# Kernel tuning notes

Measured on AMD Instinct MI355X. Metric: run time of the kernel, lower is better.

Reference implementation:

```python
import jax, jax.numpy as jnp
import numpy as np

NORM_EPS = 1e-5
NUM_HEAD = 16
DIM_HEAD = 32
DIM_HIDDEN = 512
DIM_POS = 2
N, S = 4, 8192


def setup_inputs() -> dict:
    key = jax.random.key(0)
    ks = jax.random.split(key, 16)
    d = DIM_HIDDEN
    inp = {
        "Q": jax.random.normal(ks[0], (N, S, d), jnp.float32),
        "K": jax.random.normal(ks[1], (N, S, d), jnp.float32),
        "V": jax.random.normal(ks[2], (N, S, d), jnp.float32),
        "position": jax.random.uniform(ks[3], (N, S, DIM_POS), jnp.float32),
        "W_Q": jax.random.normal(ks[4], (d, d), jnp.float32) * (1.0 / np.sqrt(d)),
        "W_K": jax.random.normal(ks[5], (d, d), jnp.float32) * (1.0 / np.sqrt(d)),
        "W_V": jax.random.normal(ks[6], (d, d), jnp.float32) * (1.0 / np.sqrt(d)),
        "b_Q": jnp.zeros((d,), jnp.float32),
        "b_K": jnp.zeros((d,), jnp.float32),
        "b_V": jnp.zeros((d,), jnp.float32),
        "ln_w_K": jnp.ones((NUM_HEAD, DIM_HEAD), jnp.float32),
        "ln_b_K": jnp.zeros((NUM_HEAD, DIM_HEAD), jnp.float32),
        "ln_w_V": jnp.ones((NUM_HEAD, DIM_HEAD), jnp.float32),
        "ln_b_V": jnp.zeros((NUM_HEAD, DIM_HEAD), jnp.float32),
        # torch Linear(dim_hidden + dim_position*num_head, dim_hidden): weight [out, in]
        "fc_W": jax.random.normal(ks[7], (d, d + DIM_POS * NUM_HEAD), jnp.float32) * (1.0 / np.sqrt(d + DIM_POS * NUM_HEAD)),
        "fc_b": jnp.zeros((d,), jnp.float32),
    }
    return inp


def _proj_heads(x, W, b):
    # [N,S,D] @ [D,D] + [D] -> [N,H,S,Dh]
    n, s, d = x.shape
    y = x @ W + b
    return y.reshape(n, s, NUM_HEAD, DIM_HEAD).transpose(0, 2, 1, 3)


def _ln(x, w, b):
    # per-head layernorm over last dim; w,b: [H,Dh] broadcast as [1,H,1,Dh]
    mu = jnp.mean(x, axis=-1, keepdims=True)
    var = jnp.mean((x - mu) ** 2, axis=-1, keepdims=True)
    xn = (x - mu) * jax.lax.rsqrt(var + NORM_EPS)
    return xn * w[None, :, None, :] + b[None, :, None, :]


def reference(Q, K, V, position, W_Q, W_K, W_V, b_Q, b_K, b_V,
              ln_w_K, ln_b_K, ln_w_V, ln_b_V, fc_W, fc_b):
    n, s, d = Q.shape
    q = _proj_heads(Q, W_Q, b_Q)                    # [N,H,S,Dh]
    k = _ln(_proj_heads(K, W_K, b_K), ln_w_K, ln_b_K)
    v = _ln(_proj_heads(V, W_V, b_V), ln_w_V, ln_b_V)
    pos = jnp.broadcast_to(position[:, None, :, :], (n, NUM_HEAD, s, DIM_POS))
    q = jnp.concatenate([pos, q], axis=-1)          # [N,H,S,P+Dh]
    k = jnp.concatenate([pos, k], axis=-1)
    v = jnp.concatenate([pos, v], axis=-1)
    # Galerkin linear attention: Q @ (K^T V / seqlen), no softmax
    ktv = jnp.einsum('nhsd,nhse->nhde', k, v) / s   # [N,H,P+Dh,P+Dh]
    x = jnp.einsum('nhsd,nhde->nhse', q, ktv)       # [N,H,S,P+Dh]
    x = x.transpose(0, 2, 1, 3).reshape(n, s, NUM_HEAD * (DIM_POS + DIM_HEAD))
    return x @ fc_W.T + fc_b
```

## Files before the change

kernel.cpp:

```cpp
#include <hip/hip_runtime.h>
#include <hip/hip_bf16.h>

typedef short short8 __attribute__((ext_vector_type(8)));
typedef float f32x4 __attribute__((ext_vector_type(4)));
typedef unsigned int uint4v __attribute__((ext_vector_type(4)));

__device__ __forceinline__ short f2bf(float f) {
  unsigned u = __builtin_bit_cast(unsigned, f);
  u += 0x7fffu + ((u >> 16) & 1u);
  return (short)(u >> 16);
}
__device__ __forceinline__ float bf2f(short s) {
  unsigned u = ((unsigned)(unsigned short)s) << 16;
  return __builtin_bit_cast(float, u);
}
__device__ __forceinline__ unsigned pk2(float a, float b) {
  __hip_bfloat162 h = __float22bfloat162_rn(float2{a, b});
  unsigned u;
  __builtin_memcpy(&u, &h, 4);
  return u;
}
__device__ __forceinline__ void gl_lds16(const void* g, void* l) {
  __builtin_amdgcn_global_load_lds(
      (const __attribute__((address_space(1))) unsigned int*)g,
      (__attribute__((address_space(3))) unsigned int*)l, 16, 0, 0);
}

__global__ __launch_bounds__(256) void wt_kernel(
    const float* __restrict__ WK, const float* __restrict__ WV,
    short* __restrict__ Wt)
{
  const int z = blockIdx.z;
  const float* W = (z == 0) ? WK : WV;
  short* o = Wt + (size_t)z * 512 * 512;
  __shared__ short t[64][65];
  const int k0 = blockIdx.y * 64, n0 = blockIdx.x * 64;
  const int c = threadIdx.x & 63, rb = threadIdx.x >> 6;
#pragma unroll
  for (int p = 0; p < 16; ++p) {
    const int kk = p * 4 + rb;
    t[kk][c] = f2bf(W[(size_t)(k0 + kk) * 512 + n0 + c]);
  }
  __syncthreads();
#pragma unroll
  for (int p = 0; p < 16; ++p) {
    const int nn = p * 4 + rb;
    o[(size_t)(n0 + nn) * 512 + k0 + c] = t[c][nn];
  }
}

__global__ __launch_bounds__(512, 2) void proj_kernel(
    const float* __restrict__ Kin, const float* __restrict__ Vin,
    const short* __restrict__ Wt,
    const float* __restrict__ bK, const float* __restrict__ bV,
    short* __restrict__ kp, short* __restrict__ vp)
{
  const int phys = blockIdx.x;
  const int log_ = (phys & 7) * 64 + (phys >> 3);
  const int z = log_ >> 8;
  const int rem = log_ & 255;
  const int row0 = (rem >> 1) * 256;
  const int col0 = (rem & 1) * 256;

  const float* X    = (z == 0) ? Kin : Vin;
  const float* bias = (z == 0) ? bK  : bV;
  const short* Wz   = Wt + (size_t)z * 512 * 512;
  short* dst        = (z == 0) ? kp : vp;

  __shared__ short a_lds[2][256 * 64];
  __shared__ short b_lds[2][256 * 64];

  const int tid = threadIdx.x;
  const int lane = tid & 63, wv = tid >> 6;
  const int wr = wv >> 2, wc = wv & 3;
  const int fr = lane & 15, fg = lane >> 4;
  const int sx = fr & 7;

  const int arow = tid >> 1, aseg = tid & 1;
  const float* abase = X + (size_t)(row0 + arow) * 512 + aseg * 32;
  int awoff[4];
#pragma unroll
  for (int m = 0; m < 4; ++m)
    awoff[m] = arow * 64 + (((aseg * 4 + m) ^ (arow & 7)) * 8);

  const int brbase = col0 + wv * 32 + (lane >> 3);
  const int bxor = ((lane & 7) ^ (lane >> 3)) * 8;
  const int bldsbase = (wv * 32) * 64;

  f32x4 acc[8][4];
#pragma unroll
  for (int i = 0; i < 8; ++i)
#pragma unroll
    for (int j = 0; j < 4; ++j) acc[i][j] = (f32x4){0.f, 0.f, 0.f, 0.f};

  f32x4 pA[8];

  {
#pragma unroll
    for (int j = 0; j < 8; ++j) pA[j] = *(const f32x4*)(abase + j * 4);
#pragma unroll
    for (int i = 0; i < 4; ++i)
      gl_lds16(Wz + (size_t)(brbase + i * 8) * 512 + bxor,
               &b_lds[0][bldsbase + i * 8 * 64]);
#pragma unroll
    for (int m = 0; m < 4; ++m) {
      uint4v s;
      s[0] = pk2(pA[2*m][0], pA[2*m][1]);     s[1] = pk2(pA[2*m][2], pA[2*m][3]);
      s[2] = pk2(pA[2*m+1][0], pA[2*m+1][1]); s[3] = pk2(pA[2*m+1][2], pA[2*m+1][3]);
      *(uint4v*)&a_lds[0][awoff[m]] = s;
    }
  }

  for (int t = 0; t < 8; ++t) {
    if (t < 7) {
      const float* ap = abase + (t + 1) * 64;
#pragma unroll
      for (int j = 0; j < 8; ++j) pA[j] = *(const f32x4*)(ap + j * 4);
      asm volatile("s_waitcnt vmcnt(8) lgkmcnt(0)" ::: "memory");
    } else {
      asm volatile("s_waitcnt vmcnt(0) lgkmcnt(0)" ::: "memory");
    }
    __builtin_amdgcn_s_barrier();
    __builtin_amdgcn_sched_barrier(0);
    if (t < 7) {
      short* bn = &b_lds[(t + 1) & 1][0];
      const int k1 = (t + 1) * 64;
#pragma unroll
      for (int i = 0; i < 4; ++i)
        gl_lds16(Wz + (size_t)(brbase + i * 8) * 512 + k1 + bxor,
                 bn + bldsbase + i * 8 * 64);
    }
    const short* ac = &a_lds[t & 1][0];
    const short* bc = &b_lds[t & 1][0];
#pragma unroll
    for (int kk = 0; kk < 2; ++kk) {
      const int so = ((kk * 4 + fg) ^ sx) * 8;
      short8 af[8], bfv[4];
#pragma unroll
      for (int ni = 0; ni < 4; ++ni)
        bfv[ni] = *(const short8*)&bc[(wc * 64 + ni * 16 + fr) * 64 + so];
#pragma unroll
      for (int mi = 0; mi < 8; ++mi)
        af[mi] = *(const short8*)&ac[(wr * 128 + mi * 16 + fr) * 64 + so];
      __builtin_amdgcn_s_setprio(1);
#pragma unroll
      for (int mi = 0; mi < 8; ++mi)
#pragma unroll
        for (int ni = 0; ni < 4; ++ni)
          acc[mi][ni] = __builtin_amdgcn_mfma_f32_16x16x32_bf16(af[mi], bfv[ni], acc[mi][ni], 0, 0, 0);
      __builtin_amdgcn_s_setprio(0);
    }
    if (t < 7) {
      short* an = &a_lds[(t + 1) & 1][0];
#pragma unroll
      for (int m = 0; m < 4; ++m) {
        uint4v s;
        s[0] = pk2(pA[2*m][0], pA[2*m][1]);     s[1] = pk2(pA[2*m][2], pA[2*m][3]);
        s[2] = pk2(pA[2*m+1][0], pA[2*m+1][1]); s[3] = pk2(pA[2*m+1][2], pA[2*m+1][3]);
        *(uint4v*)&an[awoff[m]] = s;
      }
    }
  }

#pragma unroll
  for (int ni = 0; ni < 4; ++ni) {
    const int gc = col0 + wc * 64 + ni * 16 + fr;
    const float bv = bias[gc];
#pragma unroll
    for (int mi = 0; mi < 8; ++mi) {
#pragma unroll
      for (int r = 0; r < 4; ++r) {
        const int gr = row0 + wr * 128 + mi * 16 + fg * 4 + r;
        dst[(size_t)gr * 512 + gc] = f2bf(acc[mi][ni][r] + bv);
      }
    }
  }
}

#define SC 256
#define TP 264

__global__ __launch_bounds__(256) void ktv_kernel(
    const short* __restrict__ kp, const short* __restrict__ vp,
    const float* __restrict__ pos,
    const float* __restrict__ lnwK, const float* __restrict__ lnbK,
    const float* __restrict__ lnwV, const float* __restrict__ lnbV,
    float* __restrict__ ktv)
{
  const int nh = blockIdx.y;
  const int n = nh >> 4, h = nh & 15;
  const int s0 = blockIdx.x * SC;
  const int tid = threadIdx.x;

  __shared__ short klds[48 * TP];
  __shared__ short vlds[48 * TP];
  __shared__ float lw[2][32], lb[2][32];

  if (tid < 32) {
    lw[0][tid] = lnwK[h * 32 + tid]; lb[0][tid] = lnbK[h * 32 + tid];
    lw[1][tid] = lnwV[h * 32 + tid]; lb[1][tid] = lnbV[h * 32 + tid];
  }
  __syncthreads();

  const size_t rowix = (size_t)n * 8192 + (s0 + tid);
  {
    const short8* src = (const short8*)(kp + rowix * 512 + h * 32);
    short8 r0 = src[0], r1 = src[1], r2 = src[2], r3 = src[3];
    float x[32];
#pragma unroll
    for (int i = 0; i < 8; ++i) { x[i] = bf2f(r0[i]); x[8+i] = bf2f(r1[i]); x[16+i] = bf2f(r2[i]); x[24+i] = bf2f(r3[i]); }
    float mu = 0.f;
#pragma unroll
    for (int i = 0; i < 32; ++i) mu += x[i];
    mu *= (1.f / 32.f);
    float var = 0.f;
#pragma unroll
    for (int i = 0; i < 32; ++i) { float d = x[i] - mu; var += d * d; }
    var *= (1.f / 32.f);
    const float rstd = rsqrtf(var + 1e-5f);
#pragma unroll
    for (int d = 0; d < 32; ++d)
      klds[d * TP + tid] = f2bf((x[d] - mu) * rstd * lw[0][d] + lb[0][d]);
  }
  {
    const short8* src = (const short8*)(vp + rowix * 512 + h * 32);
    short8 r0 = src[0], r1 = src[1], r2 = src[2], r3 = src[3];
    float x[32];
#pragma unroll
    for (int i = 0; i < 8; ++i) { x[i] = bf2f(r0[i]); x[8+i] = bf2f(r1[i]); x[16+i] = bf2f(r2[i]); x[24+i] = bf2f(r3[i]); }
    float mu = 0.f;
#pragma unroll
    for (int i = 0; i < 32; ++i) mu += x[i];
    mu *= (1.f / 32.f);
    float var = 0.f;
#pragma unroll
    for (int i = 0; i < 32; ++i) { float d = x[i] - mu; var += d * d; }
    var *= (1.f / 32.f);
    const float rstd = rsqrtf(var + 1e-5f);
#pragma unroll
    for (int d = 0; d < 32; ++d)
      vlds[d * TP + tid] = f2bf((x[d] - mu) * rstd * lw[1][d] + lb[1][d]);
  }
  {
    const short p0 = f2bf(pos[rowix * 2]);
    const short p1 = f2bf(pos[rowix * 2 + 1]);
    klds[32 * TP + tid] = p0; klds[33 * TP + tid] = p1;
    vlds[32 * TP + tid] = p0; vlds[33 * TP + tid] = p1;
  }
  __syncthreads();

  const int wv = tid >> 6, lane = tid & 63;
  if (wv < 3) {
    const int fr = lane & 15, fg = lane >> 4;
    f32x4 acc[3];
#pragma unroll
    for (int i = 0; i < 3; ++i) acc[i] = (f32x4){0.f, 0.f, 0.f, 0.f};
    for (int kk = 0; kk < SC; kk += 32) {
      short8 a = *(const short8*)&klds[(wv * 16 + fr) * TP + kk + fg * 8];
#pragma unroll
      for (int ni = 0; ni < 3; ++ni) {
        short8 b = *(const short8*)&vlds[(ni * 16 + fr) * TP + kk + fg * 8];
        acc[ni] = __builtin_amdgcn_mfma_f32_16x16x32_bf16(a, b, acc[ni], 0, 0, 0);
      }
    }
#pragma unroll
    for (int ni = 0; ni < 3; ++ni) {
      const int ei = ni * 16 + fr;
      if (ei < 34) {
        const int er = (ei < 32) ? ei + 2 : ei - 32;
#pragma unroll
        for (int r = 0; r < 4; ++r) {
          const int di = wv * 16 + fg * 4 + r;
          if (di < 34) {
            const int dr = (di < 32) ? di + 2 : di - 32;
            atomicAdd(&ktv[((size_t)nh * 34 + dr) * 34 + er], acc[ni][r]);
          }
        }
      }
    }
  }
}

__global__ __launch_bounds__(256) void sbuild_kernel(
    const float* __restrict__ ktv, const float* __restrict__ fcW,
    const float* __restrict__ bQ, float* __restrict__ St, float* __restrict__ Pp3)
{
  const int nh = blockIdx.x;
  const int n = nh >> 4, h = nh & 15;
  __shared__ float g[34 * 34];
  __shared__ float bq[32];
  for (int i = threadIdx.x; i < 34 * 34; i += 256)
    g[i] = ktv[(size_t)nh * 34 * 34 + i] * (1.f / 8192.f);
  if (threadIdx.x < 32) bq[threadIdx.x] = bQ[h * 32 + threadIdx.x];
  __syncthreads();

  for (int o = threadIdx.x; o < 512; o += 256) {
    float wcol[34];
#pragma unroll
    for (int e = 0; e < 34; ++e) wcol[e] = fcW[(size_t)o * 544 + h * 34 + e];
    float p0 = 0.f, p1 = 0.f;
#pragma unroll
    for (int e = 0; e < 34; ++e) { p0 += g[e] * wcol[e]; p1 += g[34 + e] * wcol[e]; }
    float rv = 0.f;
    float* srow = St + ((size_t)n * 512 + o) * 512 + h * 32;
#pragma unroll
    for (int j = 0; j < 32; ++j) {
      float s = 0.f;
#pragma unroll
      for (int e = 0; e < 34; ++e) s += g[(j + 2) * 34 + e] * wcol[e];
      srow[j] = s;
      rv += bq[j] * s;
    }
    atomicAdd(&Pp3[((size_t)n * 3 + 0) * 512 + o], p0);
    atomicAdd(&Pp3[((size_t)n * 3 + 1) * 512 + o], p1);
    atomicAdd(&Pp3[((size_t)n * 3 + 2) * 512 + o], rv);
  }
}

__global__ __launch_bounds__(256) void cbuild_kernel(
    const float* __restrict__ St, const float* __restrict__ WQ,
    short* __restrict__ Ct)
{
  const int n = blockIdx.z;
  const int row0 = blockIdx.y * 128;
  const int col0 = blockIdx.x * 128;
  const float* A = St + (size_t)n * 512 * 512;
  const float* B = WQ;

  __shared__ short a_lds[128 * 32];
  __shared__ short b_lds[128 * 32];

  const int tid = threadIdx.x;
  const int lane = tid & 63, wv = tid >> 6;
  const int wr = wv >> 1, wc = wv & 1;
  const int fr = lane & 15, fg = lane >> 4;
  const int ar = tid >> 1, ak = (tid & 1) * 16;

  f32x4 acc[4][4];
#pragma unroll
  for (int i = 0; i < 4; ++i)
#pragma unroll
    for (int j = 0; j < 4; ++j) acc[i][j] = (f32x4){0.f, 0.f, 0.f, 0.f};

  for (int k0 = 0; k0 < 512; k0 += 32) {
    __syncthreads();
    {
      const f32x4* ap = (const f32x4*)(A + (size_t)(row0 + ar) * 512 + k0 + ak);
      f32x4 f0 = ap[0], f1 = ap[1], f2 = ap[2], f3 = ap[3];
      uint4v s0, s1;
      s0[0] = pk2(f0[0], f0[1]); s0[1] = pk2(f0[2], f0[3]);
      s0[2] = pk2(f1[0], f1[1]); s0[3] = pk2(f1[2], f1[3]);
      s1[0] = pk2(f2[0], f2[1]); s1[1] = pk2(f2[2], f2[3]);
      s1[2] = pk2(f3[0], f3[1]); s1[3] = pk2(f3[2], f3[3]);
      *(uint4v*)&a_lds[ar * 32 + ak] = s0;
      *(uint4v*)&a_lds[ar * 32 + ak + 8] = s1;
      const f32x4* bp = (const f32x4*)(B + (size_t)(col0 + ar) * 512 + k0 + ak);
      f32x4 g0 = bp[0], g1 = bp[1], g2 = bp[2], g3 = bp[3];
      s0[0] = pk2(g0[0], g0[1]); s0[1] = pk2(g0[2], g0[3]);
      s0[2] = pk2(g1[0], g1[1]); s0[3] = pk2(g1[2], g1[3]);
      s1[0] = pk2(g2[0], g2[1]); s1[1] = pk2(g2[2], g2[3]);
      s1[2] = pk2(g3[0], g3[1]); s1[3] = pk2(g3[2], g3[3]);
      *(uint4v*)&b_lds[ar * 32 + ak] = s0;
      *(uint4v*)&b_lds[ar * 32 + ak + 8] = s1;
    }
    __syncthreads();

    short8 af[4], bfr[4];
#pragma unroll
    for (int mi = 0; mi < 4; ++mi)
      af[mi] = *(const short8*)&a_lds[(wr * 64 + mi * 16 + fr) * 32 + fg * 8];
#pragma unroll
    for (int ni = 0; ni < 4; ++ni)
      bfr[ni] = *(const short8*)&b_lds[(wc * 64 + ni * 16 + fr) * 32 + fg * 8];
#pragma unroll
    for (int mi = 0; mi < 4; ++mi)
#pragma unroll
      for (int ni = 0; ni < 4; ++ni)
        acc[mi][ni] = __builtin_amdgcn_mfma_f32_16x16x32_bf16(af[mi], bfr[ni], acc[mi][ni], 0, 0, 0);
  }

#pragma unroll
  for (int ni = 0; ni < 4; ++ni) {
    const int gc = col0 + wc * 64 + ni * 16 + fr;
#pragma unroll
    for (int mi = 0; mi < 4; ++mi)
#pragma unroll
      for (int r = 0; r < 4; ++r) {
        const int gr = row0 + wr * 64 + mi * 16 + fg * 4 + r;
        Ct[((size_t)n * 512 + gr) * 512 + gc] = f2bf(acc[mi][ni][r]);
      }
  }
}

__global__ __launch_bounds__(512, 2) void fuse_kernel(
    const float* __restrict__ Q, const short* __restrict__ Ct,
    const float* __restrict__ pos, const float* __restrict__ Pp3,
    const float* __restrict__ fcb, float* __restrict__ out)
{
  const int phys = blockIdx.x;
  const int log_ = (phys & 7) * 32 + (phys >> 3);
  const int n = log_ >> 6;
  const int rem = log_ & 63;
  const int row0 = (rem >> 1) * 256;
  const int col0 = (rem & 1) * 256;

  const float* X = Q + (size_t)n * 8192 * 512;
  const short* Bz = Ct + (size_t)n * 512 * 512;

  __shared__ short a_lds[2][256 * 64];
  __shared__ short b_lds[2][256 * 64];

  const int tid = threadIdx.x;
  const int lane = tid & 63, wv = tid >> 6;
  const int wr = wv >> 2, wc = wv & 3;
  const int fr = lane & 15, fg = lane >> 4;
  const int sx = fr & 7;

  const int arow = tid >> 1, aseg = tid & 1;
  const float* abase = X + (size_t)(row0 + arow) * 512 + aseg * 32;
  int awoff[4];
#pragma unroll
  for (int m = 0; m < 4; ++m)
    awoff[m] = arow * 64 + (((aseg * 4 + m) ^ (arow & 7)) * 8);

  const int brbase = col0 + wv * 32 + (lane >> 3);
  const int bxor = ((lane & 7) ^ (lane >> 3)) * 8;
  const int bldsbase = (wv * 32) * 64;

  f32x4 acc[8][4];
#pragma unroll
  for (int i = 0; i < 8; ++i)
#pragma unroll
    for (int j = 0; j < 4; ++j) acc[i][j] = (f32x4){0.f, 0.f, 0.f, 0.f};

  f32x4 pA[8];

  {
#pragma unroll
    for (int j = 0; j < 8; ++j) pA[j] = *(const f32x4*)(abase + j * 4);
#pragma unroll
    for (int i = 0; i < 4; ++i)
      gl_lds16(Bz + (size_t)(brbase + i * 8) * 512 + bxor,
               &b_lds[0][bldsbase + i * 8 * 64]);
#pragma unroll
    for (int m = 0; m < 4; ++m) {
      uint4v s;
      s[0] = pk2(pA[2*m][0], pA[2*m][1]);     s[1] = pk2(pA[2*m][2], pA[2*m][3]);
      s[2] = pk2(pA[2*m+1][0], pA[2*m+1][1]); s[3] = pk2(pA[2*m+1][2], pA[2*m+1][3]);
      *(uint4v*)&a_lds[0][awoff[m]] = s;
    }
  }

  for (int t = 0; t < 8; ++t) {
    if (t < 7) {
      const float* ap = abase + (t + 1) * 64;
#pragma unroll
      for (int j = 0; j < 8; ++j) pA[j] = *(const f32x4*)(ap + j * 4);
      asm volatile("s_waitcnt vmcnt(8) lgkmcnt(0)" ::: "memory");
    } else {
      asm volatile("s_waitcnt vmcnt(0) lgkmcnt(0)" ::: "memory");
    }
    __builtin_amdgcn_s_barrier();
    __builtin_amdgcn_sched_barrier(0);
    if (t < 7) {
      short* bn = &b_lds[(t + 1) & 1][0];
      const int k1 = (t + 1) * 64;
#pragma unroll
      for (int i = 0; i < 4; ++i)
        gl_lds16(Bz + (size_t)(brbase + i * 8) * 512 + k1 + bxor,
                 bn + bldsbase + i * 8 * 64);
    }
    const short* ac = &a_lds[t & 1][0];
    const short* bc = &b_lds[t & 1][0];
#pragma unroll
    for (int kk = 0; kk < 2; ++kk) {
      const int so = ((kk * 4 + fg) ^ sx) * 8;
      short8 af[8], bfv[4];
#pragma unroll
      for (int ni = 0; ni < 4; ++ni)
        bfv[ni] = *(const short8*)&bc[(wc * 64 + ni * 16 + fr) * 64 + so];
#pragma unroll
      for (int mi = 0; mi < 8; ++mi)
        af[mi] = *(const short8*)&ac[(wr * 128 + mi * 16 + fr) * 64 + so];
      __builtin_amdgcn_s_setprio(1);
#pragma unroll
      for (int mi = 0; mi < 8; ++mi)
#pragma unroll
        for (int ni = 0; ni < 4; ++ni)
          acc[mi][ni] = __builtin_amdgcn_mfma_f32_16x16x32_bf16(af[mi], bfv[ni], acc[mi][ni], 0, 0, 0);
      __builtin_amdgcn_s_setprio(0);
    }
    if (t < 7) {
      short* an = &a_lds[(t + 1) & 1][0];
#pragma unroll
      for (int m = 0; m < 4; ++m) {
        uint4v s;
        s[0] = pk2(pA[2*m][0], pA[2*m][1]);     s[1] = pk2(pA[2*m][2], pA[2*m][3]);
        s[2] = pk2(pA[2*m+1][0], pA[2*m+1][1]); s[3] = pk2(pA[2*m+1][2], pA[2*m+1][3]);
        *(uint4v*)&an[awoff[m]] = s;
      }
    }
  }

  float pp0[4], pp1[4], rv[4];
#pragma unroll
  for (int ni = 0; ni < 4; ++ni) {
    const int gc = col0 + wc * 64 + ni * 16 + fr;
    pp0[ni] = Pp3[((size_t)n * 3 + 0) * 512 + gc];
    pp1[ni] = Pp3[((size_t)n * 3 + 1) * 512 + gc];
    rv[ni]  = Pp3[((size_t)n * 3 + 2) * 512 + gc] + fcb[gc];
  }
#pragma unroll
  for (int mi = 0; mi < 8; ++mi) {
#pragma unroll
    for (int r = 0; r < 4; ++r) {
      const int gr = row0 + wr * 128 + mi * 16 + fg * 4 + r;
      const float* pr = pos + ((size_t)n * 8192 + gr) * 2;
      const float q0 = pr[0], q1 = pr[1];
#pragma unroll
      for (int ni = 0; ni < 4; ++ni) {
        const int gc = col0 + wc * 64 + ni * 16 + fr;
        out[((size_t)n * 8192 + gr) * 512 + gc] =
            acc[mi][ni][r] + pp0[ni] * q0 + pp1[ni] * q1 + rv[ni];
      }
    }
  }
}

extern "C" void kernel_launch(void* const* d_in, const int* in_sizes, int n_in,
                              void* d_out, int out_size, void* d_ws, size_t ws_size,
                              hipStream_t stream) {
  const float* Q    = (const float*)d_in[0];
  const float* Kin  = (const float*)d_in[1];
  const float* Vin  = (const float*)d_in[2];
  const float* pos  = (const float*)d_in[3];
  const float* WQ   = (const float*)d_in[4];
  const float* WK   = (const float*)d_in[5];
  const float* WV   = (const float*)d_in[6];
  const float* bQ   = (const float*)d_in[7];
  const float* bK   = (const float*)d_in[8];
  const float* bV   = (const float*)d_in[9];
  const float* lnwK = (const float*)d_in[10];
  const float* lnbK = (const float*)d_in[11];
  const float* lnwV = (const float*)d_in[12];
  const float* lnbV = (const float*)d_in[13];
  const float* fcW  = (const float*)d_in[14];
  const float* fcb  = (const float*)d_in[15];

  char* ws = (char*)d_ws;
  const size_t KP_B  = (size_t)4 * 8192 * 512 * 2;
  const size_t KTV_B = (size_t)64 * 34 * 34 * 4;
  const size_t ST_B  = (size_t)4 * 512 * 512 * 4;
  const size_t CT_B  = (size_t)4 * 512 * 512 * 2;
  const size_t WT_B  = (size_t)2 * 512 * 512 * 2;
  const size_t PP_B  = (size_t)4 * 3 * 512 * 4;
  short* kp  = (short*)ws;
  short* vp  = (short*)(ws + KP_B);
  float* ktv = (float*)(ws + 2 * KP_B);
  float* St  = (float*)(ws + 2 * KP_B + KTV_B);
  short* Ct  = (short*)(ws + 2 * KP_B + KTV_B + ST_B);
  short* Wt  = (short*)(ws + 2 * KP_B + KTV_B + ST_B + CT_B);
  float* Pp3 = (float*)(ws + 2 * KP_B + KTV_B + ST_B + CT_B + WT_B);

  (void)hipMemsetAsync(ktv, 0, KTV_B, stream);
  (void)hipMemsetAsync(Pp3, 0, PP_B, stream);
  hipLaunchKernelGGL(wt_kernel, dim3(8, 8, 2), dim3(256), 0, stream, WK, WV, Wt);
  hipLaunchKernelGGL(proj_kernel, dim3(512), dim3(512), 0, stream,
                     Kin, Vin, Wt, bK, bV, kp, vp);
  hipLaunchKernelGGL(ktv_kernel, dim3(32, 64), dim3(256), 0, stream,
                     kp, vp, pos, lnwK, lnbK, lnwV, lnbV, ktv);
  hipLaunchKernelGGL(sbuild_kernel, dim3(64), dim3(256), 0, stream,
                     ktv, fcW, bQ, St, Pp3);
  hipLaunchKernelGGL(cbuild_kernel, dim3(4, 4, 4), dim3(256), 0, stream,
                     St, WQ, Ct);
  hipLaunchKernelGGL(fuse_kernel, dim3(256), dim3(512), 0, stream,
                     Q, Ct, pos, Pp3, fcb, (float*)d_out);
}
```

Before: 223.4 us.

## Restructure GEMM main loops into quarter-tile phases and split sbuild grid

The proj and fuse GEMM kernels' K-loops are reorganised into four sub-tile phases per K-step. Global loads, bf16 conversion and LDS stores for the next stage are interleaved between MFMA groups, with barriers around each phase. The loader mapping changes to four threads per row covering two 128-row halves, and the B loads are split accordingly. Separately, sbuild_kernel gets a 4-way grid split over the j dimension for more parallelism, at the cost of recomputing the fcW column loads per block and extra atomics.

```diff
diff --git a/kernel.cpp b/kernel.cpp
--- a/kernel.cpp
+++ b/kernel.cpp
@@ -24,6 +24,15 @@
   __builtin_amdgcn_global_load_lds(
       (const __attribute__((address_space(1))) unsigned int*)g,
       (__attribute__((address_space(3))) unsigned int*)l, 16, 0, 0);
+}
+__device__ __forceinline__ void cvt16(const f32x4* p, short* d0, short* d1) {
+  uint4v s;
+  s[0] = pk2(p[0][0], p[0][1]); s[1] = pk2(p[0][2], p[0][3]);
+  s[2] = pk2(p[1][0], p[1][1]); s[3] = pk2(p[1][2], p[1][3]);
+  *(uint4v*)d0 = s;
+  s[0] = pk2(p[2][0], p[2][1]); s[1] = pk2(p[2][2], p[2][3]);
+  s[2] = pk2(p[3][0], p[3][1]); s[3] = pk2(p[3][2], p[3][3]);
+  *(uint4v*)d1 = s;
 }
 
 __global__ __launch_bounds__(256) void wt_kernel(
@@ -74,18 +83,16 @@
   const int lane = tid & 63, wv = tid >> 6;
   const int wr = wv >> 2, wc = wv & 3;
   const int fr = lane & 15, fg = lane >> 4;
-  const int sx = fr & 7;
-
-  const int arow = tid >> 1, aseg = tid & 1;
-  const float* abase = X + (size_t)(row0 + arow) * 512 + aseg * 32;
-  int awoff[4];
-#pragma unroll
-  for (int m = 0; m < 4; ++m)
-    awoff[m] = arow * 64 + (((aseg * 4 + m) ^ (arow & 7)) * 8);
-
-  const int brbase = col0 + wv * 32 + (lane >> 3);
-  const int bxor = ((lane & 7) ^ (lane >> 3)) * 8;
-  const int bldsbase = (wv * 32) * 64;
+  const int sxm = fr & 7;
+
+  const int arow = tid >> 2, aseg = tid & 3;
+  const float* abase = X + (size_t)(row0 + arow) * 512 + aseg * 16;
+  const int awo0 = arow * 64 + (((aseg * 2 + 0) ^ (arow & 7)) * 8);
+  const int awo1 = arow * 64 + (((aseg * 2 + 1) ^ (arow & 7)) * 8);
+
+  const int brr = wv * 16 + (lane >> 3);
+  const int bso = ((lane & 7) ^ ((lane >> 3) & 7)) * 8;
+  const int bdo = (wv * 16) * 64 + lane * 8;
 
   f32x4 acc[8][4];
 #pragma unroll
@@ -93,71 +100,84 @@
 #pragma unroll
     for (int j = 0; j < 4; ++j) acc[i][j] = (f32x4){0.f, 0.f, 0.f, 0.f};
 
-  f32x4 pA[8];
+  f32x4 pA0[4], pA1[4];
 
   {
 #pragma unroll
-    for (int j = 0; j < 8; ++j) pA[j] = *(const f32x4*)(abase + j * 4);
-#pragma unroll
-    for (int i = 0; i < 4; ++i)
-      gl_lds16(Wz + (size_t)(brbase + i * 8) * 512 + bxor,
-               &b_lds[0][bldsbase + i * 8 * 64]);
-#pragma unroll
-    for (int m = 0; m < 4; ++m) {
-      uint4v s;
-      s[0] = pk2(pA[2*m][0], pA[2*m][1]);     s[1] = pk2(pA[2*m][2], pA[2*m][3]);
-      s[2] = pk2(pA[2*m+1][0], pA[2*m+1][1]); s[3] = pk2(pA[2*m+1][2], pA[2*m+1][3]);
-      *(uint4v*)&a_lds[0][awoff[m]] = s;
-    }
-  }
-
-  for (int t = 0; t < 8; ++t) {
-    if (t < 7) {
-      const float* ap = abase + (t + 1) * 64;
-#pragma unroll
-      for (int j = 0; j < 8; ++j) pA[j] = *(const f32x4*)(ap + j * 4);
-      asm volatile("s_waitcnt vmcnt(8) lgkmcnt(0)" ::: "memory");
-    } else {
-      asm volatile("s_waitcnt vmcnt(0) lgkmcnt(0)" ::: "memory");
-    }
-    __builtin_amdgcn_s_barrier();
-    __builtin_amdgcn_sched_barrier(0);
-    if (t < 7) {
-      short* bn = &b_lds[(t + 1) & 1][0];
-      const int k1 = (t + 1) * 64;
-#pragma unroll
-      for (int i = 0; i < 4; ++i)
-        gl_lds16(Wz + (size_t)(brbase + i * 8) * 512 + k1 + bxor,
-                 bn + bldsbase + i * 8 * 64);
-    }
-    const short* ac = &a_lds[t & 1][0];
-    const short* bc = &b_lds[t & 1][0];
-#pragma unroll
-    for (int kk = 0; kk < 2; ++kk) {
-      const int so = ((kk * 4 + fg) ^ sx) * 8;
-      short8 af[8], bfv[4];
-#pragma unroll
-      for (int ni = 0; ni < 4; ++ni)
-        bfv[ni] = *(const short8*)&bc[(wc * 64 + ni * 16 + fr) * 64 + so];
-#pragma unroll
-      for (int mi = 0; mi < 8; ++mi)
-        af[mi] = *(const short8*)&ac[(wr * 128 + mi * 16 + fr) * 64 + so];
-      __builtin_amdgcn_s_setprio(1);
-#pragma unroll
-      for (int mi = 0; mi < 8; ++mi)
-#pragma unroll
-        for (int ni = 0; ni < 4; ++ni)
-          acc[mi][ni] = __builtin_amdgcn_mfma_f32_16x16x32_bf16(af[mi], bfv[ni], acc[mi][ni], 0, 0, 0);
-      __builtin_amdgcn_s_setprio(0);
-    }
-    if (t < 7) {
-      short* an = &a_lds[(t + 1) & 1][0];
-#pragma unroll
-      for (int m = 0; m < 4; ++m) {
-        uint4v s;
-        s[0] = pk2(pA[2*m][0], pA[2*m][1]);     s[1] = pk2(pA[2*m][2], pA[2*m][3]);
-        s[2] = pk2(pA[2*m+1][0], pA[2*m+1][1]); s[3] = pk2(pA[2*m+1][2], pA[2*m+1][3]);
-        *(uint4v*)&an[awoff[m]] = s;
+    for (int hh = 0; hh < 2; ++hh)
+#pragma unroll
+      for (int j = 0; j < 2; ++j)
+        gl_lds16(Wz + (size_t)(col0 + hh * 128 + brr + j * 8) * 512 + bso,
+                 &b_lds[0][bdo + (hh * 128 + j * 8) * 64]);
+#pragma unroll
+    for (int j = 0; j < 4; ++j) pA0[j] = *(const f32x4*)(abase + j * 4);
+#pragma unroll
+    for (int j = 0; j < 4; ++j) pA1[j] = *(const f32x4*)(abase + (size_t)128 * 512 + j * 4);
+    cvt16(pA0, &a_lds[0][awo0], &a_lds[0][awo1]);
+    cvt16(pA1, &a_lds[0][awo0 + 128 * 64], &a_lds[0][awo1 + 128 * 64]);
+  }
+  asm volatile("s_waitcnt lgkmcnt(0)" ::: "memory");
+  __builtin_amdgcn_s_barrier();
+
+  for (int i = 0; i < 4; ++i) {
+#pragma unroll
+    for (int h = 0; h < 2; ++h) {
+      const int st = 2 * i + h + 1;
+      const bool dost = (st < 8);
+      const int sb = st & 1;
+      const short* ab = &a_lds[h][0];
+      const short* bb = &b_lds[h][0];
+#pragma unroll
+      for (int q = 0; q < 4; ++q) {
+        short8 af[2][4], bf[2][2];
+#pragma unroll
+        for (int kk = 0; kk < 2; ++kk) {
+          const int so = (((kk << 2) | fg) ^ sxm) * 8;
+#pragma unroll
+          for (int ni = 0; ni < 2; ++ni)
+            bf[kk][ni] = *(const short8*)&bb[(wc * 64 + (q & 1) * 32 + ni * 16 + fr) * 64 + so];
+#pragma unroll
+          for (int mi = 0; mi < 4; ++mi)
+            af[kk][mi] = *(const short8*)&ab[(wr * 128 + (q >> 1) * 64 + mi * 16 + fr) * 64 + so];
+        }
+        bool wrote = false;
+        if (dost) {
+          if (q == 0) {
+#pragma unroll
+            for (int hh = 0; hh < 2; ++hh)
+#pragma unroll
+              for (int j = 0; j < 2; ++j)
+                gl_lds16(Wz + (size_t)(col0 + hh * 128 + brr + j * 8) * 512 + st * 64 + bso,
+                         &b_lds[sb][bdo + (hh * 128 + j * 8) * 64]);
+#pragma unroll
+            for (int j = 0; j < 4; ++j)
+              pA0[j] = *(const f32x4*)(abase + st * 64 + j * 4);
+          } else if (q == 1) {
+#pragma unroll
+            for (int j = 0; j < 4; ++j)
+              pA1[j] = *(const f32x4*)(abase + (size_t)128 * 512 + st * 64 + j * 4);
+          } else if (q == 2) {
+            cvt16(pA0, &a_lds[sb][awo0], &a_lds[sb][awo1]);
+            wrote = true;
+          } else {
+            cvt16(pA1, &a_lds[sb][awo0 + 128 * 64], &a_lds[sb][awo1 + 128 * 64]);
+            wrote = true;
+          }
+        }
+        if (wrote) asm volatile("s_waitcnt lgkmcnt(0)" ::: "memory");
+        __builtin_amdgcn_s_barrier();
+        __builtin_amdgcn_s_setprio(1);
+#pragma unroll
+        for (int kk = 0; kk < 2; ++kk)
+#pragma unroll
+          for (int mi = 0; mi < 4; ++mi)
+#pragma unroll
+            for (int ni = 0; ni < 2; ++ni)
+              acc[(q >> 1) * 4 + mi][(q & 1) * 2 + ni] =
+                  __builtin_amdgcn_mfma_f32_16x16x32_bf16(
+                      af[kk][mi], bf[kk][ni], acc[(q >> 1) * 4 + mi][(q & 1) * 2 + ni], 0, 0, 0);
+        __builtin_amdgcn_s_setprio(0);
+        __builtin_amdgcn_s_barrier();
       }
     }
   }
@@ -287,33 +307,37 @@
 {
   const int nh = blockIdx.x;
   const int n = nh >> 4, h = nh & 15;
+  const int jq = blockIdx.y;
   __shared__ float g[34 * 34];
-  __shared__ float bq[32];
+  __shared__ float bq8[8];
   for (int i = threadIdx.x; i < 34 * 34; i += 256)
     g[i] = ktv[(size_t)nh * 34 * 34 + i] * (1.f / 8192.f);
-  if (threadIdx.x < 32) bq[threadIdx.x] = bQ[h * 32 + threadIdx.x];
+  if (threadIdx.x < 8) bq8[threadIdx.x] = bQ[h * 32 + jq * 8 + threadIdx.x];
   __syncthreads();
 
   for (int o = threadIdx.x; o < 512; o += 256) {
     float wcol[34];
 #pragma unroll
     for (int e = 0; e < 34; ++e) wcol[e] = fcW[(size_t)o * 544 + h * 34 + e];
-    float p0 = 0.f, p1 = 0.f;
-#pragma unroll
-    for (int e = 0; e < 34; ++e) { p0 += g[e] * wcol[e]; p1 += g[34 + e] * wcol[e]; }
     float rv = 0.f;
-    float* srow = St + ((size_t)n * 512 + o) * 512 + h * 32;
-#pragma unroll
-    for (int j = 0; j < 32; ++j) {
+    float* srow = St + ((size_t)n * 512 + o) * 512 + h * 32 + jq * 8;
+#pragma unroll
+    for (int jj = 0; jj < 8; ++jj) {
+      const int j = jq * 8 + jj;
       float s = 0.f;
 #pragma unroll
       for (int e = 0; e < 34; ++e) s += g[(j + 2) * 34 + e] * wcol[e];
-      srow[j] = s;
-      rv += bq[j] * s;
-    }
-    atomicAdd(&Pp3[((size_t)n * 3 + 0) * 512 + o], p0);
-    atomicAdd(&Pp3[((size_t)n * 3 + 1) * 512 + o], p1);
+      srow[jj] = s;
+      rv += bq8[jj] * s;
+    }
     atomicAdd(&Pp3[((size_t)n * 3 + 2) * 512 + o], rv);
+    if (jq == 0) {
+      float p0 = 0.f, p1 = 0.f;
+#pragma unroll
+      for (int e = 0; e < 34; ++e) { p0 += g[e] * wcol[e]; p1 += g[34 + e] * wcol[e]; }
+      atomicAdd(&Pp3[((size_t)n * 3 + 0) * 512 + o], p0);
+      atomicAdd(&Pp3[((size_t)n * 3 + 1) * 512 + o], p1);
+    }
   }
 }
 
@@ -414,18 +438,16 @@
   const int lane = tid & 63, wv = tid >> 6;
   const int wr = wv >> 2, wc = wv & 3;
   const int fr = lane & 15, fg = lane >> 4;
-  const int sx = fr & 7;
-
-  const int arow = tid >> 1, aseg = tid & 1;
-  const float* abase = X + (size_t)(row0 + arow) * 512 + aseg * 32;
-  int awoff[4];
-#pragma unroll
-  for (int m = 0; m < 4; ++m)
-    awoff[m] = arow * 64 + (((aseg * 4 + m) ^ (arow & 7)) * 8);
-
-  const int brbase = col0 + wv * 32 + (lane >> 3);
-  const int bxor = ((lane & 7) ^ (lane >> 3)) * 8;
-  const int bldsbase = (wv * 32) * 64;
+  const int sxm = fr & 7;
+
+  const int arow = tid >> 2, aseg = tid & 3;
+  const float* abase = X + (size_t)(row0 + arow) * 512 + aseg * 16;
+  const int awo0 = arow * 64 + (((aseg * 2 + 0) ^ (arow & 7)) * 8);
+  const int awo1 = arow * 64 + (((aseg * 2 + 1) ^ (arow & 7)) * 8);
+
+  const int brr = wv * 16 + (lane >> 3);
+  const int bso = ((lane & 7) ^ ((lane >> 3) & 7)) * 8;
+  const int bdo = (wv * 16) * 64 + lane * 8;
 
   f32x4 acc[8][4];
 #pragma unroll
@@ -433,71 +455,84 @@
 #pragma unroll
     for (int j = 0; j < 4; ++j) acc[i][j] = (f32x4){0.f, 0.f, 0.f, 0.f};
 
-  f32x4 pA[8];
+  f32x4 pA0[4], pA1[4];
 
   {
 #pragma unroll
-    for (int j = 0; j < 8; ++j) pA[j] = *(const f32x4*)(abase + j * 4);
-#pragma unroll
-    for (int i = 0; i < 4; ++i)
-      gl_lds16(Bz + (size_t)(brbase + i * 8) * 512 + bxor,
-               &b_lds[0][bldsbase + i * 8 * 64]);
-#pragma unroll
-    for (int m = 0; m < 4; ++m) {
-      uint4v s;
-      s[0] = pk2(pA[2*m][0], pA[2*m][1]);     s[1] = pk2(pA[2*m][2], pA[2*m][3]);
-      s[2] = pk2(pA[2*m+1][0], pA[2*m+1][1]); s[3] = pk2(pA[2*m+1][2], pA[2*m+1][3]);
-      *(uint4v*)&a_lds[0][awoff[m]] = s;
-    }
-  }
-
-  for (int t = 0; t < 8; ++t) {
-    if (t < 7) {
-      const float* ap = abase + (t + 1) * 64;
-#pragma unroll
-      for (int j = 0; j < 8; ++j) pA[j] = *(const f32x4*)(ap + j * 4);
-      asm volatile("s_waitcnt vmcnt(8) lgkmcnt(0)" ::: "memory");
-    } else {
-      asm volatile("s_waitcnt vmcnt(0) lgkmcnt(0)" ::: "memory");
-    }
-    __builtin_amdgcn_s_barrier();
-    __builtin_amdgcn_sched_barrier(0);
-    if (t < 7) {
-      short* bn = &b_lds[(t + 1) & 1][0];
-      const int k1 = (t + 1) * 64;
-#pragma unroll
-      for (int i = 0; i < 4; ++i)
-        gl_lds16(Bz + (size_t)(brbase + i * 8) * 512 + k1 + bxor,
-                 bn + bldsbase + i * 8 * 64);
-    }
-    const short* ac = &a_lds[t & 1][0];
-    const short* bc = &b_lds[t & 1][0];
-#pragma unroll
-    for (int kk = 0; kk < 2; ++kk) {
-      const int so = ((kk * 4 + fg) ^ sx) * 8;
-      short8 af[8], bfv[4];
-#pragma unroll
-      for (int ni = 0; ni < 4; ++ni)
-        bfv[ni] = *(const short8*)&bc[(wc * 64 + ni * 16 + fr) * 64 + so];
-#pragma unroll
-      for (int mi = 0; mi < 8; ++mi)
-        af[mi] = *(const short8*)&ac[(wr * 128 + mi * 16 + fr) * 64 + so];
-      __builtin_amdgcn_s_setprio(1);
-#pragma unroll
-      for (int mi = 0; mi < 8; ++mi)
-#pragma unroll
-        for (int ni = 0; ni < 4; ++ni)
-          acc[mi][ni] = __builtin_amdgcn_mfma_f32_16x16x32_bf16(af[mi], bfv[ni], acc[mi][ni], 0, 0, 0);
-      __builtin_amdgcn_s_setprio(0);
-    }
-    if (t < 7) {
-      short* an = &a_lds[(t + 1) & 1][0];
-#pragma unroll
-      for (int m = 0; m < 4; ++m) {
-        uint4v s;
-        s[0] = pk2(pA[2*m][0], pA[2*m][1]);     s[1] = pk2(pA[2*m][2], pA[2*m][3]);
-        s[2] = pk2(pA[2*m+1][0], pA[2*m+1][1]); s[3] = pk2(pA[2*m+1][2], pA[2*m+1][3]);
-        *(uint4v*)&an[awoff[m]] = s;
+    for (int hh = 0; hh < 2; ++hh)
+#pragma unroll
+      for (int j = 0; j < 2; ++j)
+        gl_lds16(Bz + (size_t)(col0 + hh * 128 + brr + j * 8) * 512 + bso,
+                 &b_lds[0][bdo + (hh * 128 + j * 8) * 64]);
+#pragma unroll
+    for (int j = 0; j < 4; ++j) pA0[j] = *(const f32x4*)(abase + j * 4);
+#pragma unroll
+    for (int j = 0; j < 4; ++j) pA1[j] = *(const f32x4*)(abase + (size_t)128 * 512 + j * 4);
+    cvt16(pA0, &a_lds[0][awo0], &a_lds[0][awo1]);
+    cvt16(pA1, &a_lds[0][awo0 + 128 * 64], &a_lds[0][awo1 + 128 * 64]);
+  }
+  asm volatile("s_waitcnt lgkmcnt(0)" ::: "memory");
+  __builtin_amdgcn_s_barrier();
+
+  for (int i = 0; i < 4; ++i) {
+#pragma unroll
+    for (int h = 0; h < 2; ++h) {
+      const int st = 2 * i + h + 1;
+      const bool dost = (st < 8);
+      const int sb = st & 1;
+      const short* ab = &a_lds[h][0];
+      const short* bb = &b_lds[h][0];
+#pragma unroll
+      for (int q = 0; q < 4; ++q) {
+        short8 af[2][4], bf[2][2];
+#pragma unroll
+        for (int kk = 0; kk < 2; ++kk) {
+          const int so = (((kk << 2) | fg) ^ sxm) * 8;
+#pragma unroll
+          for (int ni = 0; ni < 2; ++ni)
+            bf[kk][ni] = *(const short8*)&bb[(wc * 64 + (q & 1) * 32 + ni * 16 + fr) * 64 + so];
+#pragma unroll
+          for (int mi = 0; mi < 4; ++mi)
+            af[kk][mi] = *(const short8*)&ab[(wr * 128 + (q >> 1) * 64 + mi * 16 + fr) * 64 + so];
+        }
+        bool wrote = false;
+        if (dost) {
+          if (q == 0) {
+#pragma unroll
+            for (int hh = 0; hh < 2; ++hh)
+#pragma unroll
+              for (int j = 0; j < 2; ++j)
+                gl_lds16(Bz + (size_t)(col0 + hh * 128 + brr + j * 8) * 512 + st * 64 + bso,
+                         &b_lds[sb][bdo + (hh * 128 + j * 8) * 64]);
+#pragma unroll
+            for (int j = 0; j < 4; ++j)
+              pA0[j] = *(const f32x4*)(abase + st * 64 + j * 4);
+          } else if (q == 1) {
+#pragma unroll
+            for (int j = 0; j < 4; ++j)
+              pA1[j] = *(const f32x4*)(abase + (size_t)128 * 512 + st * 64 + j * 4);
+          } else if (q == 2) {
+            cvt16(pA0, &a_lds[sb][awo0], &a_lds[sb][awo1]);
+            wrote = true;
+          } else {
+            cvt16(pA1, &a_lds[sb][awo0 + 128 * 64], &a_lds[sb][awo1 + 128 * 64]);
+            wrote = true;
+          }
+        }
+        if (wrote) asm volatile("s_waitcnt lgkmcnt(0)" ::: "memory");
+        __builtin_amdgcn_s_barrier();
+        __builtin_amdgcn_s_setprio(1);
+#pragma unroll
+        for (int kk = 0; kk < 2; ++kk)
+#pragma unroll
+          for (int mi = 0; mi < 4; ++mi)
+#pragma unroll
+            for (int ni = 0; ni < 2; ++ni)
+              acc[(q >> 1) * 4 + mi][(q & 1) * 2 + ni] =
+                  __builtin_amdgcn_mfma_f32_16x16x32_bf16(
+                      af[kk][mi], bf[kk][ni], acc[(q >> 1) * 4 + mi][(q & 1) * 2 + ni], 0, 0, 0);
+        __builtin_amdgcn_s_setprio(0);
+        __builtin_amdgcn_s_barrier();
       }
     }
   }
@@ -569,7 +604,7 @@
                      Kin, Vin, Wt, bK, bV, kp, vp);
   hipLaunchKernelGGL(ktv_kernel, dim3(32, 64), dim3(256), 0, stream,
                      kp, vp, pos, lnwK, lnbK, lnwV, lnbV, ktv);
-  hipLaunchKernelGGL(sbuild_kernel, dim3(64), dim3(256), 0, stream,
+  hipLaunchKernelGGL(sbuild_kernel, dim3(64, 4), dim3(256), 0, stream,
                      ktv, fcW, bQ, St, Pp3);
   hipLaunchKernelGGL(cbuild_kernel, dim3(4, 4, 4), dim3(256), 0, stream,
                      St, WQ, Ct);
```

Result: faster. 200.2 us (-10.4%).
